# Kernel optimization log

Measured on AMD Instinct MI355X. Metric: run time of the kernel, lower is better.

Reference implementation:

```python
import jax, jax.numpy as jnp
import numpy as np

B, T, F, H, V = 32, 512, 128, 2048, 32
INPUT_INT_SCALE = 7.0
G_RES = 1.0
G_IN = 1.0


def setup_inputs() -> dict:
    key = jax.random.key(0)
    ks = jax.random.split(key, 7)
    x = jax.random.normal(ks[0], (B, T, F), dtype=jnp.float32)
    # int4 weights in [-7, 7] (randint 0..15 shifted by -7, clipped to -7)
    W_res_i4 = jnp.clip(jax.random.randint(ks[1], (H, H), 0, 15, dtype=jnp.int32) - 7, -7, 7)
    W_in_i4 = jnp.clip(jax.random.randint(ks[2], (H, F), 0, 15, dtype=jnp.int32) - 7, -7, 7)
    # positive per-row dequant scales
    S_res_row = jax.random.uniform(ks[3], (H,), dtype=jnp.float32, minval=0.5, maxval=1.5)
    S_in_row = jax.random.uniform(ks[4], (H,), dtype=jnp.float32, minval=0.5, maxval=1.5)
    W_out_w = jax.random.normal(ks[5], (V, H), dtype=jnp.float32) / np.sqrt(H).astype(np.float32)
    W_out_b = jnp.zeros((V,), dtype=jnp.float32)
    return {"x": x, "W_res_i4": W_res_i4, "W_in_i4": W_in_i4,
            "S_res_row": S_res_row, "S_in_row": S_in_row,
            "W_out_w": W_out_w, "W_out_b": W_out_b}


def reference(x, W_res_i4, W_in_i4, S_res_row, S_in_row, W_out_w, W_out_b):
    # Row scales: s_res = S_res/49 * g_res ; s_in = S_in/(7*max(1,scale)) * g_in
    s_res = (S_res_row / 49.0 * G_RES)[None, :]                       # (1,H)
    s_in = (S_in_row / (7.0 * max(1.0, INPUT_INT_SCALE)) * G_IN)[None, :]
    Wr_T = W_res_i4.T  # (H,H): y[b,i] = sum_j W[i,j] * h[b,j] -> h @ W.T
    Wi_T = W_in_i4.T   # (F,H)

    def step(h, x_t):
        # quantize input and state
        u_int = jnp.round(x_t * INPUT_INT_SCALE).astype(jnp.int32)        # (B,F)
        h_int = jnp.round(jnp.clip(h, -1.0, 1.0) * 7.0).astype(jnp.int32)  # (B,H)
        # int matvecs + int16 clamp + dequant
        out_res = jnp.clip(h_int @ Wr_T, -32768, 32767).astype(jnp.float32)  # (B,H)
        out_in = jnp.clip(u_int @ Wi_T, -32768, 32767).astype(jnp.float32)   # (B,H)
        h_new = jnp.tanh(out_res * s_res + out_in * s_in)
        return h_new, h_new

    h0 = jnp.zeros((x.shape[0], H), dtype=jnp.float32)
    _, hs = jax.lax.scan(step, h0, jnp.swapaxes(x, 0, 1))  # (T,B,H)
    Hs = jnp.swapaxes(hs, 0, 1)                            # (B,T,H)
    return Hs @ W_out_w.T + W_out_b                        # (B,T,V)
```

## Files before the change

kernel.cpp:

```cpp
#include <hip/hip_runtime.h>
#include <hip/hip_bf16.h>

typedef __attribute__((ext_vector_type(2))) int   i32x2;
typedef __attribute__((ext_vector_type(4))) int   i32x4;
typedef __attribute__((ext_vector_type(4))) float f32x4;
typedef __attribute__((ext_vector_type(4))) short s16x4;
typedef __attribute__((ext_vector_type(8))) short s16x8;

#define B_  32
#define T_  512
#define F_  128
#define H_  2048
#define V_  32
#define NBLK_ 64

static __device__ __forceinline__ int clampi16(int v) {
  v = v < -32768 ? -32768 : v;
  return v > 32767 ? 32767 : v;
}
static __device__ __forceinline__ short f2bf(float f) {
  union { __hip_bfloat16 b; short s; } u; u.b = __float2bfloat16(f); return u.s;
}
static __device__ __forceinline__ s16x8 as_s16x8(i32x4 v) {
  union { i32x4 i; s16x8 s; } u; u.i = v; return u.s;
}
static __device__ __forceinline__ s16x4 as_s16x4(i32x2 v) {
  union { i32x2 i; s16x4 s; } u; u.i = v; return u.s;
}
static __device__ __forceinline__ i32x2 as_i32x2(s16x4 v) {
  union { s16x4 s; i32x2 i; } u; u.s = v; return u.i;
}

static __device__ __forceinline__ float xla_tanh_fma(float x) {
#pragma clang fp contract(off)
  const float kClamp = 7.90531110763549805f;
  float xc = fminf(fmaxf(x, -kClamp), kClamp);
  float x2 = xc * xc;
  float a;
  a = -2.76076847742355e-16f;
  a = __builtin_fmaf(a, x2, 2.00018790482477e-13f);
  a = __builtin_fmaf(a, x2, -8.60467152213735e-11f);
  a = __builtin_fmaf(a, x2, 5.12229709037114e-08f);
  a = __builtin_fmaf(a, x2, 1.48572235717979e-05f);
  a = __builtin_fmaf(a, x2, 6.37261928875436e-04f);
  a = __builtin_fmaf(a, x2, 4.89352455891786e-03f);
  float num = xc * a;
  float b;
  b = 1.19825839466702e-06f;
  b = __builtin_fmaf(b, x2, 1.18534705686654e-04f);
  b = __builtin_fmaf(b, x2, 2.26843463243900e-03f);
  b = __builtin_fmaf(b, x2, 4.89352518554385e-03f);
  float r = num / b;
  return (fabsf(x) < 0.0004f) ? x : r;
}

__global__ __launch_bounds__(256) void pack_k(const int* __restrict__ Wr4,
                                              const int* __restrict__ Wi4,
                                              const float* __restrict__ Wo,
                                              short* __restrict__ WrB,
                                              short* __restrict__ WiB,
                                              short* __restrict__ WoB) {
  const int idx = blockIdx.x * 256 + threadIdx.x;
  {
    i32x4 v = *(const i32x4*)(Wr4 + (size_t)idx * 4);
    s16x4 o;
#pragma unroll
    for (int r = 0; r < 4; ++r) o[r] = f2bf((float)v[r]);
    *(s16x4*)(WrB + (size_t)idx * 4) = o;
  }
  if (idx < (H_ * F_ / 4)) {
    i32x4 v = *(const i32x4*)(Wi4 + (size_t)idx * 4);
    s16x4 o;
#pragma unroll
    for (int r = 0; r < 4; ++r) o[r] = f2bf((float)v[r]);
    *(s16x4*)(WiB + (size_t)idx * 4) = o;
  }
  if (idx < (V_ * H_ / 4)) {
    f32x4 f = *(const f32x4*)(Wo + (size_t)idx * 4);
    s16x4 o;
#pragma unroll
    for (int r = 0; r < 4; ++r) o[r] = f2bf(f[r]);
    *(s16x4*)(WoB + (size_t)idx * 4) = o;
  }
}

__global__ __launch_bounds__(256) void in_gemm(const float* __restrict__ x,
                                               const short* __restrict__ WiB,
                                               short* __restrict__ Oin) {
  const int t  = blockIdx.x;
  const int jt = blockIdx.y;
  const int tid = threadIdx.x;
  const int l = tid & 63, w = tid >> 6;
  const int mh = w & 1, q = w >> 1;
  const int lr = l & 15, lc = l >> 4;
  const int brow = mh * 16 + lr;

  s16x8 af[4];
  const float* xp = x + ((size_t)brow * T_ + t) * F_;
#pragma unroll
  for (int kk = 0; kk < 4; ++kk) {
    f32x4 f0 = *(const f32x4*)(xp + kk * 32 + lc * 8);
    f32x4 f1 = *(const f32x4*)(xp + kk * 32 + lc * 8 + 4);
    s16x8 a;
#pragma unroll
    for (int c = 0; c < 4; ++c) a[c]     = f2bf(rintf(f0[c] * 7.0f));
#pragma unroll
    for (int c = 0; c < 4; ++c) a[4 + c] = f2bf(rintf(f1[c] * 7.0f));
    af[kk] = a;
  }
#pragma unroll
  for (int s = 0; s < 4; ++s) {
    const int j = jt * 128 + q * 64 + s * 16 + lr;
    f32x4 acc = {0.f, 0.f, 0.f, 0.f};
#pragma unroll
    for (int kk = 0; kk < 4; ++kk) {
      s16x8 b = *(const s16x8*)(WiB + (size_t)j * F_ + kk * 32 + lc * 8);
      acc = __builtin_amdgcn_mfma_f32_16x16x32_bf16(af[kk], b, acc, 0, 0, 0);
    }
    short* op = Oin + ((size_t)t * H_ + j) * B_ + mh * 16 + lc * 4;
    s16x4 ov;
#pragma unroll
    for (int r = 0; r < 4; ++r) ov[r] = (short)clampi16((int)acc[r]);
    *(s16x4*)op = ov;
  }
}

__global__ __launch_bounds__(256, 1) void recur_pers(const short* __restrict__ WrB,
                                                     const short* __restrict__ Oin,
                                                     const float* __restrict__ Sres,
                                                     const float* __restrict__ Sin,
                                                     short* __restrict__ Hb,
                                                     short* __restrict__ Hs,
                                                     int* __restrict__ barcnt) {
#pragma clang fp contract(off)
  __shared__ short hqt[32][36];
  __shared__ short hst[32][36];
  __shared__ f32x4 xch[2][2][64];

  const int tid = threadIdx.x;
  const int l = tid & 63, w = tid >> 6;
  const int mh = w & 1, nh = w >> 1;
  const int lr = l & 15, lc = l >> 4;
  const int jloc = nh * 16 + lr;
  const int jl = blockIdx.x * 32 + jloc;
  const int b0 = mh * 16;
  const int jblk = blockIdx.x * 32;

  const float RC49 = 1.0f / 49.0f;
  const float sres = Sres[jl] * RC49;
  const float sinl = Sin[jl]  * RC49;

  const short* wrow0 = WrB + (size_t)(jblk + lr) * H_      + nh * 1024 + lc * 8;
  const short* wrow1 = WrB + (size_t)(jblk + 16 + lr) * H_ + nh * 1024 + lc * 8;
  s16x8 wreg0[32], wreg1[32];
#pragma unroll
  for (int kk = 0; kk < 32; ++kk) {
    wreg0[kk] = *(const s16x8*)(wrow0 + kk * 32);
    asm volatile("" : "+v"(wreg0[kk]));
    wreg1[kk] = *(const s16x8*)(wrow1 + kk * 32);
    asm volatile("" : "+v"(wreg1[kk]));
  }

  const int bs = tid >> 3;
  const int cs = tid & 7;

  asm volatile("s_waitcnt vmcnt(0)" ::: "memory");
  __builtin_amdgcn_sched_barrier(0);

  for (int t = 0; t < T_; ++t) {
    const short* hrow = Hb + (t & 1) * (B_ * H_)
                      + (size_t)(b0 + lr) * H_ + nh * 1024 + lc * 8;
    short* hout = Hb + ((t + 1) & 1) * (B_ * H_);

    i32x2 oinr;
    {
      const short* op = Oin + ((size_t)t * H_ + jl) * B_ + b0 + lc * 4;
      asm volatile("global_load_dwordx2 %0, %1, off"
                   : "=v"(oinr) : "v"(op) : "memory");
    }
    i32x4 a[32];
#pragma unroll
    for (int i = 0; i < 32; ++i)
      asm volatile("global_load_dwordx4 %0, %1, off offset:%2 sc0 sc1"
                   : "=v"(a[i]) : "v"(hrow), "n"(i * 64) : "memory");

    f32x4 accE0 = {0.f, 0.f, 0.f, 0.f}, accO0 = {0.f, 0.f, 0.f, 0.f};
    f32x4 accE1 = {0.f, 0.f, 0.f, 0.f}, accO1 = {0.f, 0.f, 0.f, 0.f};

    asm volatile("s_waitcnt vmcnt(16)" ::: "memory");
    __builtin_amdgcn_sched_barrier(0);
#pragma unroll
    for (int i = 0; i < 16; i += 2) {
      accE0 = __builtin_amdgcn_mfma_f32_16x16x32_bf16(as_s16x8(a[i]),     wreg0[i],     accE0, 0, 0, 0);
      accE1 = __builtin_amdgcn_mfma_f32_16x16x32_bf16(as_s16x8(a[i]),     wreg1[i],     accE1, 0, 0, 0);
      accO0 = __builtin_amdgcn_mfma_f32_16x16x32_bf16(as_s16x8(a[i + 1]), wreg0[i + 1], accO0, 0, 0, 0);
      accO1 = __builtin_amdgcn_mfma_f32_16x16x32_bf16(as_s16x8(a[i + 1]), wreg1[i + 1], accO1, 0, 0, 0);
    }
    asm volatile("s_waitcnt vmcnt(0)" ::: "memory");
    __builtin_amdgcn_sched_barrier(0);
#pragma unroll
    for (int i = 16; i < 32; i += 2) {
      accE0 = __builtin_amdgcn_mfma_f32_16x16x32_bf16(as_s16x8(a[i]),     wreg0[i],     accE0, 0, 0, 0);
      accE1 = __builtin_amdgcn_mfma_f32_16x16x32_bf16(as_s16x8(a[i]),     wreg1[i],     accE1, 0, 0, 0);
      accO0 = __builtin_amdgcn_mfma_f32_16x16x32_bf16(as_s16x8(a[i + 1]), wreg0[i + 1], accO0, 0, 0, 0);
      accO1 = __builtin_amdgcn_mfma_f32_16x16x32_bf16(as_s16x8(a[i + 1]), wreg1[i + 1], accO1, 0, 0, 0);
    }

    f32x4 own0, own1;
#pragma unroll
    for (int r = 0; r < 4; ++r) { own0[r] = accE0[r] + accO0[r]; own1[r] = accE1[r] + accO1[r]; }
    xch[mh][1 - nh][l] = (nh == 0) ? own1 : own0;
    __syncthreads();
    const f32x4 part = xch[mh][nh][l];
    const f32x4 mine = (nh == 0) ? own0 : own1;

    const s16x4 oin = as_s16x4(oinr);
#pragma unroll
    for (int r = 0; r < 4; ++r) {
      const int b = b0 + lc * 4 + r;
      const float resf = mine[r] + part[r];
      const int   res  = clampi16((int)resf);
      const float t2   = (float)oin[r] * sinl;
      const float z    = __builtin_fmaf((float)res, sres, t2);
      const float h    = xla_tanh_fma(z);
      const float hc   = fminf(fmaxf(h, -1.0f), 1.0f);
      hqt[b][jloc] = f2bf(rintf(hc * 7.0f));
      hst[b][jloc] = f2bf(h);
    }

    __syncthreads();

    {
      const i32x2 hqv = as_i32x2(*(const s16x4*)&hqt[bs][cs * 4]);
      const i32x2 hsv = as_i32x2(*(const s16x4*)&hst[bs][cs * 4]);
      short* hq_dst = hout + (size_t)bs * H_ + jblk + cs * 4;
      short* hs_dst = Hs + ((size_t)bs * T_ + t) * H_ + jblk + cs * 4;
      asm volatile("global_store_dwordx2 %0, %1, off sc0 sc1"
                   :: "v"(hq_dst), "v"(hqv) : "memory");
      asm volatile("global_store_dwordx2 %0, %1, off"
                   :: "v"(hs_dst), "v"(hsv) : "memory");
    }

    if (t != T_ - 1) {
      asm volatile("s_waitcnt vmcnt(0)" ::: "memory");
      __syncthreads();
      if (tid == 0) {
        __hip_atomic_fetch_add(&barcnt[(blockIdx.x & 7) * 32], 1,
                               __ATOMIC_RELAXED, __HIP_MEMORY_SCOPE_AGENT);
        const int target = NBLK_ * (t + 1);
        for (;;) {
          int s = 0;
#pragma unroll
          for (int i = 0; i < 8; ++i)
            s += __hip_atomic_load(&barcnt[i * 32], __ATOMIC_RELAXED,
                                   __HIP_MEMORY_SCOPE_AGENT);
          if (s >= target) break;
          __builtin_amdgcn_s_sleep(1);
        }
        asm volatile("s_waitcnt vmcnt(0)" ::: "memory");
      }
      __syncthreads();
    }
  }
}

__global__ __launch_bounds__(256, 1) void diag_bar(int* __restrict__ bar2) {
  const int tid = threadIdx.x;
  for (int t = 0; t < 128; ++t) {
    __syncthreads();
    if (tid == 0) {
      __hip_atomic_fetch_add(&bar2[(blockIdx.x & 7) * 32], 1,
                             __ATOMIC_RELAXED, __HIP_MEMORY_SCOPE_AGENT);
      const int target = NBLK_ * (t + 1);
      for (;;) {
        int s = 0;
#pragma unroll
        for (int i = 0; i < 8; ++i)
          s += __hip_atomic_load(&bar2[i * 32], __ATOMIC_RELAXED,
                                 __HIP_MEMORY_SCOPE_AGENT);
        if (s >= target) break;
        __builtin_amdgcn_s_sleep(1);
      }
      asm volatile("s_waitcnt vmcnt(0)" ::: "memory");
    }
    __syncthreads();
  }
}

__global__ __launch_bounds__(256) void out_gemm(const unsigned short* __restrict__ Hs,
                                                const unsigned short* __restrict__ WoB,
                                                const float* __restrict__ bias,
                                                float* __restrict__ out) {
  const int tid = threadIdx.x;
  const int l = tid & 63, w = tid >> 6;
  const int m0 = blockIdx.x * 64 + w * 16;
  const int lr = l & 15, lc = l >> 4;

  f32x4 acc0 = {0.f, 0.f, 0.f, 0.f}, acc1 = {0.f, 0.f, 0.f, 0.f};
  const unsigned short* arow = Hs  + (size_t)(m0 + lr) * H_ + lc * 8;
  const unsigned short* bp0  = WoB + (size_t)lr * H_        + lc * 8;
  const unsigned short* bp1  = WoB + (size_t)(16 + lr) * H_ + lc * 8;
#pragma unroll 8
  for (int kk = 0; kk < 64; ++kk) {
    s16x8 a  = *(const s16x8*)(arow + kk * 32);
    s16x8 b0 = *(const s16x8*)(bp0  + kk * 32);
    s16x8 b1 = *(const s16x8*)(bp1  + kk * 32);
    acc0 = __builtin_amdgcn_mfma_f32_16x16x32_bf16(a, b0, acc0, 0, 0, 0);
    acc1 = __builtin_amdgcn_mfma_f32_16x16x32_bf16(a, b1, acc1, 0, 0, 0);
  }
#pragma unroll
  for (int r = 0; r < 4; ++r) {
    const int m = m0 + lc * 4 + r;
    out[(size_t)m * V_ + lr]      = acc0[r] + bias[lr];
    out[(size_t)m * V_ + 16 + lr] = acc1[r] + bias[16 + lr];
  }
}

extern "C" void kernel_launch(void* const* d_in, const int* in_sizes, int n_in,
                              void* d_out, int out_size, void* d_ws, size_t ws_size,
                              hipStream_t stream) {
  if (n_in != 7) return;
  const int exp_sz[7] = {B_ * T_ * F_, H_ * H_, H_ * F_, H_, H_, V_ * H_, V_};
  for (int i = 0; i < 7; ++i) if (in_sizes[i] != exp_sz[i]) return;

  const float* x    = (const float*)d_in[0];
  const int*   Wr4  = (const int*)d_in[1];
  const int*   Wi4  = (const int*)d_in[2];
  const float* Sres = (const float*)d_in[3];
  const float* Sin  = (const float*)d_in[4];
  const float* Wo   = (const float*)d_in[5];
  const float* Wob  = (const float*)d_in[6];
  float* out = (float*)d_out;
  char* ws = (char*)d_ws;

  const size_t OFF_WRB = 0;
  const size_t OFF_WIB = 8388608;
  const size_t OFF_WOB = 8912896;
  const size_t OFF_OIN = 9043968;
  const size_t OFF_HS  = 76152832;
  const size_t OFF_HB  = 143261696;
  const size_t OFF_BAR = 143523840;
  const size_t OFF_BR2 = 143524864;
  const size_t NEED    = 143525888;
  if (ws_size < NEED) return;

  short* WrB = (short*)(ws + OFF_WRB);
  short* WiB = (short*)(ws + OFF_WIB);
  short* WoB = (short*)(ws + OFF_WOB);
  short* Oin = (short*)(ws + OFF_OIN);
  short* HsP = (short*)(ws + OFF_HS);
  short* Hb  = (short*)(ws + OFF_HB);
  int*   Bar = (int*)(ws + OFF_BAR);
  int*   Br2 = (int*)(ws + OFF_BR2);

  hipMemsetAsync(Hb, 0, B_ * H_ * 2, stream);
  hipMemsetAsync(Bar, 0, 2048, stream);

  pack_k<<<dim3(H_ * H_ / (4 * 256)), dim3(256), 0, stream>>>(Wr4, Wi4, Wo, WrB, WiB, WoB);
  in_gemm<<<dim3(T_, H_ / 128), dim3(256), 0, stream>>>(x, WiB, Oin);

  recur_pers<<<dim3(NBLK_), dim3(256), 0, stream>>>(WrB, Oin, Sres, Sin, Hb, HsP, Bar);

  out_gemm<<<dim3(256), dim3(256), 0, stream>>>((const unsigned short*)HsP,
                                                (const unsigned short*)WoB, Wob, out);

  diag_bar<<<dim3(NBLK_), dim3(256), 0, stream>>>(Br2);
}
```

Measured before the change: 4.393 ms.

## Replace counter grid barrier with per-block step flags and drop diagnostic kernel

Replaces the atomic-counter grid barrier in the persistent recurrence kernel with per-block flags. Each block publishes its completed step with one atomic store. Before loading the hidden state for the next step, each wave spins with every lane polling one block's flag. This removes the atomic add, the eight-slot sum poll and a trailing __syncthreads, and the wait now overlaps the already-issued Oin load. It also removes the separate diag_bar barrier-timing kernel from the launch sequence. The cost is more polling traffic, since every wave of every block polls all 64 flags, and correctness now relies on the relaxed-ordering assumptions around the flag store.

```diff
diff --git a/kernel.cpp b/kernel.cpp
--- a/kernel.cpp
+++ b/kernel.cpp
@@ -131,7 +131,7 @@
                                                      const float* __restrict__ Sin,
                                                      short* __restrict__ Hb,
                                                      short* __restrict__ Hs,
-                                                     int* __restrict__ barcnt) {
+                                                     int* __restrict__ flags) {
 #pragma clang fp contract(off)
   __shared__ short hqt[32][36];
   __shared__ short hst[32][36];
@@ -178,6 +178,16 @@
       asm volatile("global_load_dwordx2 %0, %1, off"
                    : "=v"(oinr) : "v"(op) : "memory");
     }
+
+    if (t != 0) {
+      for (;;) {
+        const int fv = __hip_atomic_load(&flags[l * 4], __ATOMIC_RELAXED,
+                                         __HIP_MEMORY_SCOPE_AGENT);
+        if (fv >= t) break;
+        __builtin_amdgcn_s_sleep(1);
+      }
+    }
+
     i32x4 a[32];
 #pragma unroll
     for (int i = 0; i < 32; ++i)
@@ -244,46 +254,10 @@
     if (t != T_ - 1) {
       asm volatile("s_waitcnt vmcnt(0)" ::: "memory");
       __syncthreads();
-      if (tid == 0) {
-        __hip_atomic_fetch_add(&barcnt[(blockIdx.x & 7) * 32], 1,
-                               __ATOMIC_RELAXED, __HIP_MEMORY_SCOPE_AGENT);
-        const int target = NBLK_ * (t + 1);
-        for (;;) {
-          int s = 0;
-#pragma unroll
-          for (int i = 0; i < 8; ++i)
-            s += __hip_atomic_load(&barcnt[i * 32], __ATOMIC_RELAXED,
-                                   __HIP_MEMORY_SCOPE_AGENT);
-          if (s >= target) break;
-          __builtin_amdgcn_s_sleep(1);
-        }
-        asm volatile("s_waitcnt vmcnt(0)" ::: "memory");
-      }
-      __syncthreads();
-    }
-  }
-}
-
-__global__ __launch_bounds__(256, 1) void diag_bar(int* __restrict__ bar2) {
-  const int tid = threadIdx.x;
-  for (int t = 0; t < 128; ++t) {
-    __syncthreads();
-    if (tid == 0) {
-      __hip_atomic_fetch_add(&bar2[(blockIdx.x & 7) * 32], 1,
-                             __ATOMIC_RELAXED, __HIP_MEMORY_SCOPE_AGENT);
-      const int target = NBLK_ * (t + 1);
-      for (;;) {
-        int s = 0;
-#pragma unroll
-        for (int i = 0; i < 8; ++i)
-          s += __hip_atomic_load(&bar2[i * 32], __ATOMIC_RELAXED,
-                                 __HIP_MEMORY_SCOPE_AGENT);
-        if (s >= target) break;
-        __builtin_amdgcn_s_sleep(1);
-      }
-      asm volatile("s_waitcnt vmcnt(0)" ::: "memory");
-    }
-    __syncthreads();
+      if (tid == 0)
+        __hip_atomic_store(&flags[blockIdx.x * 4], t + 1,
+                           __ATOMIC_RELAXED, __HIP_MEMORY_SCOPE_AGENT);
+    }
   }
 }
 
@@ -339,9 +313,8 @@
   const size_t OFF_OIN = 9043968;
   const size_t OFF_HS  = 76152832;
   const size_t OFF_HB  = 143261696;
-  const size_t OFF_BAR = 143523840;
-  const size_t OFF_BR2 = 143524864;
-  const size_t NEED    = 143525888;
+  const size_t OFF_FLG = 143523840;
+  const size_t NEED    = 143524864;
   if (ws_size < NEED) return;
 
   short* WrB = (short*)(ws + OFF_WRB);
@@ -350,19 +323,16 @@
   short* Oin = (short*)(ws + OFF_OIN);
   short* HsP = (short*)(ws + OFF_HS);
   short* Hb  = (short*)(ws + OFF_HB);
-  int*   Bar = (int*)(ws + OFF_BAR);
-  int*   Br2 = (int*)(ws + OFF_BR2);
+  int*   Flg = (int*)(ws + OFF_FLG);
 
   hipMemsetAsync(Hb, 0, B_ * H_ * 2, stream);
-  hipMemsetAsync(Bar, 0, 2048, stream);
+  hipMemsetAsync(Flg, 0, 1024, stream);
 
   pack_k<<<dim3(H_ * H_ / (4 * 256)), dim3(256), 0, stream>>>(Wr4, Wi4, Wo, WrB, WiB, WoB);
   in_gemm<<<dim3(T_, H_ / 128), dim3(256), 0, stream>>>(x, WiB, Oin);
 
-  recur_pers<<<dim3(NBLK_), dim3(256), 0, stream>>>(WrB, Oin, Sres, Sin, Hb, HsP, Bar);
+  recur_pers<<<dim3(NBLK_), dim3(256), 0, stream>>>(WrB, Oin, Sres, Sin, Hb, HsP, Flg);
 
   out_gemm<<<dim3(256), dim3(256), 0, stream>>>((const unsigned short*)HsP,
                                                 (const unsigned short*)WoB, Wob, out);
-
-  diag_bar<<<dim3(NBLK_), dim3(256), 0, stream>>>(Br2);
-}
+}
```

After: 3.572 ms. -18.7%, faster.
